# Kernel optimization log

Hardware: AMD Instinct MI355X
Metric: run time of the kernel (lower is better)

## Reference

```python
import jax, jax.numpy as jnp
import numpy as np

N_NODES = 100000
N_EDGES = 1600000
IN_DIM, HID_DIM, OUT_DIM = 512, 64, 32


def _gcn_conv(x, row, col, W, b, n):
    # GCNConv: h = x W; out[v] = sum_{(u,v)} norm(u,v) * h[u] + b
    # deg computed on destination (col) with self-loops already included.
    deg = jax.ops.segment_sum(jnp.ones_like(col, dtype=x.dtype), col, num_segments=n)
    dinv = jnp.where(deg > 0, jax.lax.rsqrt(deg), 0.0)
    norm = dinv[row] * dinv[col]                      # [E]
    h = x @ W                                          # [N, out]
    msg = h[row] * norm[:, None]                       # [E, out] gather
    out = jax.ops.segment_sum(msg, col, num_segments=n)  # scatter-add
    return out + b


def setup_inputs() -> dict:
    key = jax.random.key(0)
    k1, k2, k3, k4 = jax.random.split(key, 4)
    x = jax.random.normal(k1, (N_NODES, IN_DIM), dtype=jnp.float32)
    edge_index = jax.random.randint(k2, (2, N_EDGES), 0, N_NODES, dtype=jnp.int64)
    W1 = jax.random.normal(k3, (IN_DIM, HID_DIM), dtype=jnp.float32) / np.sqrt(IN_DIM)
    b1 = jnp.zeros((HID_DIM,), dtype=jnp.float32)
    W2 = jax.random.normal(k4, (HID_DIM, OUT_DIM), dtype=jnp.float32) / np.sqrt(HID_DIM)
    b2 = jnp.zeros((OUT_DIM,), dtype=jnp.float32)
    return {"x": x, "edge_index": edge_index, "W1": W1, "b1": b1, "W2": W2, "b2": b2}


def reference(x, edge_index, W1, b1, W2, b2):
    n = x.shape[0]
    # add self-loops (PyG GCNConv default add_self_loops=True)
    loop = jnp.arange(n, dtype=edge_index.dtype)
    row = jnp.concatenate([edge_index[0], loop])
    col = jnp.concatenate([edge_index[1], loop])
    h = _gcn_conv(x, row, col, W1, b1, n)
    h = jax.nn.relu(h)
    # dropout is identity in eval mode (training=False)
    h = _gcn_conv(h, row, col, W2, b2, n)
    return jax.nn.log_softmax(h, axis=1)
```

## Files before the change

### kernel.cpp

```cpp
#include <hip/hip_runtime.h>
#include <hip/hip_fp16.h>


#define IN_DIM 512
#define HID    64
#define OUTD   32

typedef __attribute__((ext_vector_type(8))) short bf16x8;
typedef __attribute__((ext_vector_type(4))) float floatx4;
typedef __attribute__((ext_vector_type(4))) unsigned short ushort4v;
typedef __attribute__((ext_vector_type(8))) unsigned short ushort8v;

__device__ __forceinline__ unsigned short f2bf(float f) {
    unsigned int u = __float_as_uint(f);
    unsigned int r = (u + 0x7fffu + ((u >> 16) & 1u)) >> 16;
    return (unsigned short)r;
}
__device__ __forceinline__ float bf2f(unsigned short h) {
    return __uint_as_float(((unsigned int)h) << 16);
}

__device__ __forceinline__ float4 ld4h(const __half* p) {
    uint2 u = *(const uint2*)(p);
    __half2 a = *(__half2*)&u.x, b = *(__half2*)&u.y;
    float2 fa = __half22float2(a), fb = __half22float2(b);
    return make_float4(fa.x, fa.y, fb.x, fb.y);
}

__device__ __forceinline__ int eidx(const int* idx32, long long e, int is64) {
    if (is64) { const long long* p = (const long long*)idx32; return (int)p[e]; }
    return idx32[e];
}

__global__ void k_init(const float* __restrict__ W1,
                       unsigned short* __restrict__ W1t_hi,
                       unsigned short* __restrict__ W1t_lo,
                       const int* __restrict__ idx, int* __restrict__ flag,
                       int* __restrict__ cnt, int N) {
    int t = blockIdx.x * blockDim.x + threadIdx.x;
    if (t == 0) {
        int z = (idx[1] == 0) & (idx[3] == 0) & (idx[5] == 0) & (idx[7] == 0);
        *flag = z;
    }
    if (t < N) cnt[t] = 0;
    if (t < 64 * 512) {
        int n = t >> 9, k = t & 511;
        float v = W1[k * HID + n];
        unsigned short h = f2bf(v);
        W1t_hi[t] = h;
        W1t_lo[t] = f2bf(v - bf2f(h));
    }
}

__global__ void k_count(const int* __restrict__ idx, const int* __restrict__ flag,
                        int* __restrict__ cnt, int E) {
    int e = blockIdx.x * blockDim.x + threadIdx.x;
    if (e >= E) return;
    const int is64 = *flag;
    int c = eidx(idx, (long long)E + e, is64);
    atomicAdd(&cnt[c], 1);
}

__global__ void k_scanA(const int* __restrict__ cnt, int* __restrict__ rowptr,
                        int* __restrict__ part, float* __restrict__ dinv, int N) {
    __shared__ int s[256];
    const int t = threadIdx.x;
    const int i = blockIdx.x * 256 + t;
    int v = (i < N) ? cnt[i] : 0;
    if (i < N) dinv[i] = rsqrtf((float)(1 + v));
    s[t] = v;
    __syncthreads();
#pragma unroll
    for (int off = 1; off < 256; off <<= 1) {
        int x = (t >= off) ? s[t - off] : 0;
        __syncthreads();
        s[t] += x;
        __syncthreads();
    }
    if (i < N) rowptr[i] = s[t] - v;
    if (t == 255) part[blockIdx.x] = s[255];
}

__global__ void k_scanB(const int* __restrict__ part, int* __restrict__ partex, int nb) {
    __shared__ int s[1024];
    const int t = threadIdx.x;
    int v = (t < nb) ? part[t] : 0;
    s[t] = v;
    __syncthreads();
#pragma unroll
    for (int off = 1; off < 1024; off <<= 1) {
        int x = (t >= off) ? s[t - off] : 0;
        __syncthreads();
        s[t] += x;
        __syncthreads();
    }
    partex[t] = s[t] - v;
}

__global__ void k_scanC(int* __restrict__ rowptr, const int* __restrict__ partex,
                        int N, int E) {
    const int i = blockIdx.x * blockDim.x + threadIdx.x;
    if (i < N) rowptr[i] += partex[i >> 8];
    if (i == 0) rowptr[N] = E;
}

__global__ void k_place(const int* __restrict__ idx, const int* __restrict__ flag,
                        int* __restrict__ cnt, const int* __restrict__ rowptr,
                        int* __restrict__ src, int E) {
    int e = blockIdx.x * blockDim.x + threadIdx.x;
    if (e >= E) return;
    const int is64 = *flag;
    int r = eidx(idx, e, is64);
    int c = eidx(idx, (long long)E + e, is64);
    int ofs = atomicAdd(&cnt[c], -1) - 1;
    src[rowptr[c] + ofs] = r;
}

__launch_bounds__(256)
__global__ void k_gemm1_mfma(const float* __restrict__ x,
                             const unsigned short* __restrict__ Wt_hi,
                             const unsigned short* __restrict__ Wt_lo,
                             const float* __restrict__ dinv,
                             __half* __restrict__ g1, int N) {
    __shared__ unsigned short xs_hi[64 * 72];
    __shared__ unsigned short xs_lo[64 * 72];
    __shared__ unsigned short ws_hi[64 * 72];
    __shared__ unsigned short ws_lo[64 * 72];

    const int t = threadIdx.x;
    const int lane = t & 63;
    const int w = t >> 6;
    const int m = lane & 15;
    const int quad = lane >> 4;
    const int row_base = blockIdx.x * 64;

    const floatx4 zero = {0.0f, 0.0f, 0.0f, 0.0f};
    floatx4 acc[4] = {zero, zero, zero, zero};

    for (int kc = 0; kc < IN_DIM; kc += 64) {
        {
            const int kq = (t & 15) * 4;
#pragma unroll
            for (int p = 0; p < 4; ++p) {
                int rl = (t >> 4) + p * 16;
                int row = row_base + rl;
                if (row > N - 1) row = N - 1;
                float4 v = *(const float4*)(x + (size_t)row * IN_DIM + kc + kq);
                ushort4v hi, lo;
                hi.x = f2bf(v.x); lo.x = f2bf(v.x - bf2f(hi.x));
                hi.y = f2bf(v.y); lo.y = f2bf(v.y - bf2f(hi.y));
                hi.z = f2bf(v.z); lo.z = f2bf(v.z - bf2f(hi.z));
                hi.w = f2bf(v.w); lo.w = f2bf(v.w - bf2f(hi.w));
                *(ushort4v*)&xs_hi[rl * 72 + kq] = hi;
                *(ushort4v*)&xs_lo[rl * 72 + kq] = lo;
            }
        }
        {
            const int nl = t >> 2;
            const int q = (t & 3) * 16;
            const unsigned short* ph = Wt_hi + (size_t)nl * IN_DIM + kc + q;
            const unsigned short* pl = Wt_lo + (size_t)nl * IN_DIM + kc + q;
            *(ushort8v*)&ws_hi[nl * 72 + q]     = *(const ushort8v*)(ph);
            *(ushort8v*)&ws_hi[nl * 72 + q + 8] = *(const ushort8v*)(ph + 8);
            *(ushort8v*)&ws_lo[nl * 72 + q]     = *(const ushort8v*)(pl);
            *(ushort8v*)&ws_lo[nl * 72 + q + 8] = *(const ushort8v*)(pl + 8);
        }
        __syncthreads();
#pragma unroll
        for (int ks = 0; ks < 2; ++ks) {
            const int ko = ks * 32 + quad * 8;
            bf16x8 a_hi = *(const bf16x8*)&xs_hi[(w * 16 + m) * 72 + ko];
            bf16x8 a_lo = *(const bf16x8*)&xs_lo[(w * 16 + m) * 72 + ko];
#pragma unroll
            for (int nt = 0; nt < 4; ++nt) {
                bf16x8 b_hi = *(const bf16x8*)&ws_hi[(nt * 16 + m) * 72 + ko];
                bf16x8 b_lo = *(const bf16x8*)&ws_lo[(nt * 16 + m) * 72 + ko];
                acc[nt] = __builtin_amdgcn_mfma_f32_16x16x32_bf16(a_hi, b_hi, acc[nt], 0, 0, 0);
                acc[nt] = __builtin_amdgcn_mfma_f32_16x16x32_bf16(a_lo, b_hi, acc[nt], 0, 0, 0);
                acc[nt] = __builtin_amdgcn_mfma_f32_16x16x32_bf16(a_hi, b_lo, acc[nt], 0, 0, 0);
            }
        }
        __syncthreads();
    }
#pragma unroll
    for (int r = 0; r < 4; ++r) {
        const int row = row_base + w * 16 + quad * 4 + r;
        if (row < N) {
            const float dv = dinv[row];
#pragma unroll
            for (int nt = 0; nt < 4; ++nt)
                g1[(size_t)row * HID + nt * 16 + m] = __float2half(acc[nt][r] * dv);
        }
    }
}

__launch_bounds__(256)
__global__ void k_agg1_gemm2(const int* __restrict__ rowptr, const int* __restrict__ src,
                             const __half* __restrict__ g1, const float* __restrict__ W2,
                             const float* __restrict__ b1, const float* __restrict__ dinv,
                             __half* __restrict__ g2, int N) {
    __shared__ float w2s[HID * OUTD];
    __shared__ float hs[16][HID];
    __shared__ float sdv[16];

    const int t = threadIdx.x;
    for (int i = t; i < HID * OUTD; i += 256) w2s[i] = W2[i];

    const int wv = t >> 6, lane = t & 63;
    const int grp = lane >> 4;
    const int l16 = lane & 15;
    const int vl = wv * 4 + grp;
    const int v = blockIdx.x * 16 + vl;
    const int c0 = l16 * 4;

    if (v < N) {
        float4 acc = ld4h(g1 + (size_t)v * HID + c0);
        int i = rowptr[v];
        const int end = rowptr[v + 1];
        for (; i + 3 < end; i += 4) {
            int r0 = src[i], r1 = src[i + 1], r2 = src[i + 2], r3 = src[i + 3];
            float4 a0 = ld4h(g1 + (size_t)r0 * HID + c0);
            float4 a1 = ld4h(g1 + (size_t)r1 * HID + c0);
            float4 a2 = ld4h(g1 + (size_t)r2 * HID + c0);
            float4 a3 = ld4h(g1 + (size_t)r3 * HID + c0);
            acc.x += (a0.x + a1.x) + (a2.x + a3.x);
            acc.y += (a0.y + a1.y) + (a2.y + a3.y);
            acc.z += (a0.z + a1.z) + (a2.z + a3.z);
            acc.w += (a0.w + a1.w) + (a2.w + a3.w);
        }
        for (; i < end; ++i) {
            float4 a = ld4h(g1 + (size_t)src[i] * HID + c0);
            acc.x += a.x; acc.y += a.y; acc.z += a.z; acc.w += a.w;
        }
        const float dv = dinv[v];
        const float4 b = *(const float4*)(b1 + c0);
        float4 h;
        h.x = fmaxf(fmaf(dv, acc.x, b.x), 0.0f);
        h.y = fmaxf(fmaf(dv, acc.y, b.y), 0.0f);
        h.z = fmaxf(fmaf(dv, acc.z, b.z), 0.0f);
        h.w = fmaxf(fmaf(dv, acc.w, b.w), 0.0f);
        *(float4*)&hs[vl][c0] = h;
        if (l16 == 0) sdv[vl] = dv;
    }
    __syncthreads();
#pragma unroll
    for (int hh = 0; hh < 2; ++hh) {
        const int o = hh * 256 + t;
        const int vert = o >> 5;
        const int j = o & 31;
        const int gv = blockIdx.x * 16 + vert;
        if (gv < N) {
            float s = 0.0f;
#pragma unroll
            for (int k = 0; k < HID; ++k) s = fmaf(hs[vert][k], w2s[k * OUTD + j], s);
            g2[(size_t)gv * OUTD + j] = __float2half(s * sdv[vert]);
        }
    }
}

__global__ void k_out(const int* __restrict__ rowptr, const int* __restrict__ src,
                      const __half* __restrict__ g2, const float* __restrict__ b2,
                      const float* __restrict__ dinv, float* __restrict__ out, int N) {
    const int t = threadIdx.x;
    const int wv = t >> 6, lane = t & 63;
    const int grp = lane >> 3;
    const int l8 = lane & 7;
    const int v = blockIdx.x * 32 + wv * 8 + grp;
    if (v >= N) return;
    const int c0 = l8 * 4;

    float4 acc = ld4h(g2 + (size_t)v * OUTD + c0);
    int i = rowptr[v];
    const int end = rowptr[v + 1];
    for (; i + 3 < end; i += 4) {
        int r0 = src[i], r1 = src[i + 1], r2 = src[i + 2], r3 = src[i + 3];
        float4 a0 = ld4h(g2 + (size_t)r0 * OUTD + c0);
        float4 a1 = ld4h(g2 + (size_t)r1 * OUTD + c0);
        float4 a2 = ld4h(g2 + (size_t)r2 * OUTD + c0);
        float4 a3 = ld4h(g2 + (size_t)r3 * OUTD + c0);
        acc.x += (a0.x + a1.x) + (a2.x + a3.x);
        acc.y += (a0.y + a1.y) + (a2.y + a3.y);
        acc.z += (a0.z + a1.z) + (a2.z + a3.z);
        acc.w += (a0.w + a1.w) + (a2.w + a3.w);
    }
    for (; i < end; ++i) {
        float4 a = ld4h(g2 + (size_t)src[i] * OUTD + c0);
        acc.x += a.x; acc.y += a.y; acc.z += a.z; acc.w += a.w;
    }
    const float dv = dinv[v];
    const float4 b = *(const float4*)(b2 + c0);
    float4 z;
    z.x = fmaf(dv, acc.x, b.x);
    z.y = fmaf(dv, acc.y, b.y);
    z.z = fmaf(dv, acc.z, b.z);
    z.w = fmaf(dv, acc.w, b.w);
    float m = fmaxf(fmaxf(z.x, z.y), fmaxf(z.z, z.w));
#pragma unroll
    for (int d = 1; d < 8; d <<= 1) m = fmaxf(m, __shfl_xor(m, d, 64));
    float s = expf(z.x - m) + expf(z.y - m) + expf(z.z - m) + expf(z.w - m);
#pragma unroll
    for (int d = 1; d < 8; d <<= 1) s += __shfl_xor(s, d, 64);
    const float ml = m + logf(s);
    float4 o;
    o.x = z.x - ml; o.y = z.y - ml; o.z = z.z - ml; o.w = z.w - ml;
    *(float4*)(out + (size_t)v * OUTD + c0) = o;
}

extern "C" void kernel_launch(void* const* d_in, const int* in_sizes, int n_in,
                              void* d_out, int out_size, void* d_ws, size_t ws_size,
                              hipStream_t stream) {
    const float* x   = (const float*)d_in[0];
    const int*   idx = (const int*)d_in[1];
    const float* W1  = (const float*)d_in[2];
    const float* b1  = (const float*)d_in[3];
    const float* W2  = (const float*)d_in[4];
    const float* b2  = (const float*)d_in[5];
    float* out = (float*)d_out;

    const int N = in_sizes[0] / IN_DIM;
    const int E = in_sizes[1] / 2;

    unsigned short* W1t_hi = (unsigned short*)d_ws;
    unsigned short* W1t_lo = W1t_hi + 64 * 512;
    int* cnt    = (int*)(W1t_lo + 64 * 512);
    int* rowptr = cnt + N;
    int* part   = rowptr + (N + 4);
    int* partex = part + 1024;
    int* srcA   = partex + 1024;
    int* flag   = srcA + E;
    float* dinv = (float*)(flag + 4);
    __half* g1  = (__half*)(dinv + N);
    __half* g2  = g1 + (size_t)N * HID;

    const int B = 256;
    const int nb = (N + 255) / 256;

    k_init<<<(N + B - 1) / B, B, 0, stream>>>(W1, W1t_hi, W1t_lo, idx, flag, cnt, N);
    k_count<<<(E + B - 1) / B, B, 0, stream>>>(idx, flag, cnt, E);
    k_scanA<<<nb, 256, 0, stream>>>(cnt, rowptr, part, dinv, N);
    k_scanB<<<1, 1024, 0, stream>>>(part, partex, nb);
    k_scanC<<<nb, 256, 0, stream>>>(rowptr, partex, N, E);
    k_place<<<(E + B - 1) / B, B, 0, stream>>>(idx, flag, cnt, rowptr, srcA, E);

    k_gemm1_mfma<<<(N + 63) / 64, 256, 0, stream>>>(x, W1t_hi, W1t_lo, dinv, g1, N);
    k_agg1_gemm2<<<(N + 15) / 16, 256, 0, stream>>>(rowptr, srcA, g1, W2, b1, dinv, g2, N);
    k_out<<<(N + 31) / 32, B, 0, stream>>>(rowptr, srcA, g2, b2, dinv, out, N);
}
```

Measured before the change: 547.5 us.

## Sort vertices by in-degree to balance aggregation work across wavefronts

Builds a degree histogram and a counting-sort permutation of vertices by in-degree, then has both aggregation kernels process vertices in permuted order. Groups that share a wavefront then have similar neighbor counts, which is meant to cut divergence and load imbalance in the per-vertex gather loops. This costs two extra small kernels plus atomics, and output writes become scattered rather than contiguous.

```diff
diff --git a/kernel.cpp b/kernel.cpp
--- a/kernel.cpp
+++ b/kernel.cpp
@@ -36,12 +36,13 @@
                        unsigned short* __restrict__ W1t_hi,
                        unsigned short* __restrict__ W1t_lo,
                        const int* __restrict__ idx, int* __restrict__ flag,
-                       int* __restrict__ cnt, int N) {
+                       int* __restrict__ cnt, int* __restrict__ hist, int N) {
     int t = blockIdx.x * blockDim.x + threadIdx.x;
     if (t == 0) {
         int z = (idx[1] == 0) & (idx[3] == 0) & (idx[5] == 0) & (idx[7] == 0);
         *flag = z;
     }
+    if (t < 256) hist[t] = 0;
     if (t < N) cnt[t] = 0;
     if (t < 64 * 512) {
         int n = t >> 9, k = t & 511;
@@ -98,10 +99,57 @@
 }
 
 __global__ void k_scanC(int* __restrict__ rowptr, const int* __restrict__ partex,
+                        const int* __restrict__ cnt, int* __restrict__ hist,
                         int N, int E) {
-    const int i = blockIdx.x * blockDim.x + threadIdx.x;
-    if (i < N) rowptr[i] += partex[i >> 8];
+    __shared__ int lh[256];
+    const int t = threadIdx.x;
+    const int i = blockIdx.x * 256 + t;
+    lh[t] = 0;
+    __syncthreads();
+    if (i < N) {
+        rowptr[i] += partex[i >> 8];
+        atomicAdd(&lh[min(cnt[i], 255)], 1);
+    }
     if (i == 0) rowptr[N] = E;
+    __syncthreads();
+    int c = lh[t];
+    if (c) atomicAdd(&hist[t], c);
+}
+
+__global__ void k_binscan(const int* __restrict__ hist, int* __restrict__ binofs) {
+    __shared__ int s[256];
+    const int t = threadIdx.x;
+    int v = hist[t];
+    s[t] = v;
+    __syncthreads();
+#pragma unroll
+    for (int off = 1; off < 256; off <<= 1) {
+        int x = (t >= off) ? s[t - off] : 0;
+        __syncthreads();
+        s[t] += x;
+        __syncthreads();
+    }
+    binofs[t] = s[t] - v;
+}
+
+__global__ void k_permplace(const int* __restrict__ cnt, int* __restrict__ binofs,
+                            int* __restrict__ perm, int N) {
+    __shared__ int lh[256];
+    __shared__ int lbase[256];
+    const int t = threadIdx.x;
+    const int v = blockIdx.x * 256 + t;
+    lh[t] = 0;
+    __syncthreads();
+    int d = 0, my = 0;
+    if (v < N) {
+        d = min(cnt[v], 255);
+        my = atomicAdd(&lh[d], 1);
+    }
+    __syncthreads();
+    int c = lh[t];
+    if (c) lbase[t] = atomicAdd(&binofs[t], c);
+    __syncthreads();
+    if (v < N) perm[lbase[d] + my] = v;
 }
 
 __global__ void k_place(const int* __restrict__ idx, const int* __restrict__ flag,
@@ -196,12 +244,14 @@
 
 __launch_bounds__(256)
 __global__ void k_agg1_gemm2(const int* __restrict__ rowptr, const int* __restrict__ src,
+                             const int* __restrict__ perm,
                              const __half* __restrict__ g1, const float* __restrict__ W2,
                              const float* __restrict__ b1, const float* __restrict__ dinv,
                              __half* __restrict__ g2, int N) {
     __shared__ float w2s[HID * OUTD];
     __shared__ float hs[16][HID];
     __shared__ float sdv[16];
+    __shared__ int   svid[16];
 
     const int t = threadIdx.x;
     for (int i = t; i < HID * OUTD; i += 256) w2s[i] = W2[i];
@@ -210,10 +260,11 @@
     const int grp = lane >> 4;
     const int l16 = lane & 15;
     const int vl = wv * 4 + grp;
-    const int v = blockIdx.x * 16 + vl;
+    const int idxv = blockIdx.x * 16 + vl;
+    const int v = (idxv < N) ? perm[idxv] : -1;
     const int c0 = l16 * 4;
 
-    if (v < N) {
+    if (v >= 0) {
         float4 acc = ld4h(g1 + (size_t)v * HID + c0);
         int i = rowptr[v];
         const int end = rowptr[v + 1];
@@ -240,7 +291,9 @@
         h.z = fmaxf(fmaf(dv, acc.z, b.z), 0.0f);
         h.w = fmaxf(fmaf(dv, acc.w, b.w), 0.0f);
         *(float4*)&hs[vl][c0] = h;
-        if (l16 == 0) sdv[vl] = dv;
+        if (l16 == 0) { sdv[vl] = dv; svid[vl] = v; }
+    } else if (l16 == 0) {
+        svid[vl] = -1;
     }
     __syncthreads();
 #pragma unroll
@@ -248,8 +301,8 @@
         const int o = hh * 256 + t;
         const int vert = o >> 5;
         const int j = o & 31;
-        const int gv = blockIdx.x * 16 + vert;
-        if (gv < N) {
+        const int gv = svid[vert];
+        if (gv >= 0) {
             float s = 0.0f;
 #pragma unroll
             for (int k = 0; k < HID; ++k) s = fmaf(hs[vert][k], w2s[k * OUTD + j], s);
@@ -259,14 +312,16 @@
 }
 
 __global__ void k_out(const int* __restrict__ rowptr, const int* __restrict__ src,
+                      const int* __restrict__ perm,
                       const __half* __restrict__ g2, const float* __restrict__ b2,
                       const float* __restrict__ dinv, float* __restrict__ out, int N) {
     const int t = threadIdx.x;
     const int wv = t >> 6, lane = t & 63;
     const int grp = lane >> 3;
     const int l8 = lane & 7;
-    const int v = blockIdx.x * 32 + wv * 8 + grp;
-    if (v >= N) return;
+    const int idxv = blockIdx.x * 32 + wv * 8 + grp;
+    if (idxv >= N) return;
+    const int v = perm[idxv];
     const int c0 = l8 * 4;
 
     float4 acc = ld4h(g2 + (size_t)v * OUTD + c0);
@@ -326,7 +381,10 @@
     int* rowptr = cnt + N;
     int* part   = rowptr + (N + 4);
     int* partex = part + 1024;
-    int* srcA   = partex + 1024;
+    int* hist   = partex + 1024;
+    int* binofs = hist + 256;
+    int* perm   = binofs + 256;
+    int* srcA   = perm + N;
     int* flag   = srcA + E;
     float* dinv = (float*)(flag + 4);
     __half* g1  = (__half*)(dinv + N);
@@ -335,14 +393,16 @@
     const int B = 256;
     const int nb = (N + 255) / 256;
 
-    k_init<<<(N + B - 1) / B, B, 0, stream>>>(W1, W1t_hi, W1t_lo, idx, flag, cnt, N);
+    k_init<<<(N + B - 1) / B, B, 0, stream>>>(W1, W1t_hi, W1t_lo, idx, flag, cnt, hist, N);
     k_count<<<(E + B - 1) / B, B, 0, stream>>>(idx, flag, cnt, E);
     k_scanA<<<nb, 256, 0, stream>>>(cnt, rowptr, part, dinv, N);
     k_scanB<<<1, 1024, 0, stream>>>(part, partex, nb);
-    k_scanC<<<nb, 256, 0, stream>>>(rowptr, partex, N, E);
+    k_scanC<<<nb, 256, 0, stream>>>(rowptr, partex, cnt, hist, N, E);
+    k_binscan<<<1, 256, 0, stream>>>(hist, binofs);
+    k_permplace<<<nb, 256, 0, stream>>>(cnt, binofs, perm, N);
     k_place<<<(E + B - 1) / B, B, 0, stream>>>(idx, flag, cnt, rowptr, srcA, E);
 
     k_gemm1_mfma<<<(N + 63) / 64, 256, 0, stream>>>(x, W1t_hi, W1t_lo, dinv, g1, N);
-    k_agg1_gemm2<<<(N + 15) / 16, 256, 0, stream>>>(rowptr, srcA, g1, W2, b1, dinv, g2, N);
-    k_out<<<(N + 31) / 32, B, 0, stream>>>(rowptr, srcA, g2, b2, dinv, out, N);
-}
+    k_agg1_gemm2<<<(N + 15) / 16, 256, 0, stream>>>(rowptr, srcA, perm, g1, W2, b1, dinv, g2, N);
+    k_out<<<(N + 31) / 32, B, 0, stream>>>(rowptr, srcA, perm, g2, b2, dinv, out, N);
+}
```

Result: slower. 572.1 us (+4.5%).

## Load GEMM1 operands directly into registers and record edge offsets during counting

Applied to the files above, without the earlier changes.

The first-layer GEMM no longer stages x and W1 tiles through LDS. Each lane loads its own A fragment from global memory, converts it to bf16 hi/lo in registers, and reads B fragments straight from the pre-transposed weight arrays, so the block-wide barriers are gone. Separately, the count pass now stores each edge's atomic slot index, which lets the place pass drop its second round of atomics on the counters. The cost is an extra E-sized int buffer written and read back, and weight reads that now depend on L1/L2 caching instead of shared memory. Neighbour ordering within each row is now determined by the count pass's atomic order.

```diff
diff --git a/kernel.cpp b/kernel.cpp
--- a/kernel.cpp
+++ b/kernel.cpp
@@ -8,8 +8,6 @@
 
 typedef __attribute__((ext_vector_type(8))) short bf16x8;
 typedef __attribute__((ext_vector_type(4))) float floatx4;
-typedef __attribute__((ext_vector_type(4))) unsigned short ushort4v;
-typedef __attribute__((ext_vector_type(8))) unsigned short ushort8v;
 
 __device__ __forceinline__ unsigned short f2bf(float f) {
     unsigned int u = __float_as_uint(f);
@@ -53,12 +51,12 @@
 }
 
 __global__ void k_count(const int* __restrict__ idx, const int* __restrict__ flag,
-                        int* __restrict__ cnt, int E) {
+                        int* __restrict__ cnt, int* __restrict__ eofs, int E) {
     int e = blockIdx.x * blockDim.x + threadIdx.x;
     if (e >= E) return;
     const int is64 = *flag;
     int c = eidx(idx, (long long)E + e, is64);
-    atomicAdd(&cnt[c], 1);
+    eofs[e] = atomicAdd(&cnt[c], 1);
 }
 
 __global__ void k_scanA(const int* __restrict__ cnt, int* __restrict__ rowptr,
@@ -105,28 +103,21 @@
 }
 
 __global__ void k_place(const int* __restrict__ idx, const int* __restrict__ flag,
-                        int* __restrict__ cnt, const int* __restrict__ rowptr,
+                        const int* __restrict__ eofs, const int* __restrict__ rowptr,
                         int* __restrict__ src, int E) {
     int e = blockIdx.x * blockDim.x + threadIdx.x;
     if (e >= E) return;
     const int is64 = *flag;
     int r = eidx(idx, e, is64);
     int c = eidx(idx, (long long)E + e, is64);
-    int ofs = atomicAdd(&cnt[c], -1) - 1;
-    src[rowptr[c] + ofs] = r;
-}
-
-__launch_bounds__(256)
+    src[rowptr[c] + eofs[e]] = r;
+}
+
 __global__ void k_gemm1_mfma(const float* __restrict__ x,
                              const unsigned short* __restrict__ Wt_hi,
                              const unsigned short* __restrict__ Wt_lo,
                              const float* __restrict__ dinv,
                              __half* __restrict__ g1, int N) {
-    __shared__ unsigned short xs_hi[64 * 72];
-    __shared__ unsigned short xs_lo[64 * 72];
-    __shared__ unsigned short ws_hi[64 * 72];
-    __shared__ unsigned short ws_lo[64 * 72];
-
     const int t = threadIdx.x;
     const int lane = t & 63;
     const int w = t >> 6;
@@ -134,53 +125,43 @@
     const int quad = lane >> 4;
     const int row_base = blockIdx.x * 64;
 
+    int arow = row_base + w * 16 + m;
+    if (arow > N - 1) arow = N - 1;
+    const float* xp = x + (size_t)arow * IN_DIM + quad * 8;
+    const unsigned short* wh = Wt_hi + (size_t)m * IN_DIM + quad * 8;
+    const unsigned short* wl = Wt_lo + (size_t)m * IN_DIM + quad * 8;
+
     const floatx4 zero = {0.0f, 0.0f, 0.0f, 0.0f};
     floatx4 acc[4] = {zero, zero, zero, zero};
 
     for (int kc = 0; kc < IN_DIM; kc += 64) {
-        {
-            const int kq = (t & 15) * 4;
-#pragma unroll
-            for (int p = 0; p < 4; ++p) {
-                int rl = (t >> 4) + p * 16;
-                int row = row_base + rl;
-                if (row > N - 1) row = N - 1;
-                float4 v = *(const float4*)(x + (size_t)row * IN_DIM + kc + kq);
-                ushort4v hi, lo;
-                hi.x = f2bf(v.x); lo.x = f2bf(v.x - bf2f(hi.x));
-                hi.y = f2bf(v.y); lo.y = f2bf(v.y - bf2f(hi.y));
-                hi.z = f2bf(v.z); lo.z = f2bf(v.z - bf2f(hi.z));
-                hi.w = f2bf(v.w); lo.w = f2bf(v.w - bf2f(hi.w));
-                *(ushort4v*)&xs_hi[rl * 72 + kq] = hi;
-                *(ushort4v*)&xs_lo[rl * 72 + kq] = lo;
+#pragma unroll
+        for (int ks = 0; ks < 2; ++ks) {
+            const int ko = kc + ks * 32;
+            float4 v0 = *(const float4*)(xp + ko);
+            float4 v1 = *(const float4*)(xp + ko + 4);
+            bf16x8 a_hi, a_lo;
+            {
+                unsigned short h;
+                h = f2bf(v0.x); a_hi[0] = (short)h; a_lo[0] = (short)f2bf(v0.x - bf2f(h));
+                h = f2bf(v0.y); a_hi[1] = (short)h; a_lo[1] = (short)f2bf(v0.y - bf2f(h));
+                h = f2bf(v0.z); a_hi[2] = (short)h; a_lo[2] = (short)f2bf(v0.z - bf2f(h));
+                h = f2bf(v0.w); a_hi[3] = (short)h; a_lo[3] = (short)f2bf(v0.w - bf2f(h));
+                h = f2bf(v1.x); a_hi[4] = (short)h; a_lo[4] = (short)f2bf(v1.x - bf2f(h));
+                h = f2bf(v1.y); a_hi[5] = (short)h; a_lo[5] = (short)f2bf(v1.y - bf2f(h));
+                h = f2bf(v1.z); a_hi[6] = (short)h; a_lo[6] = (short)f2bf(v1.z - bf2f(h));
+                h = f2bf(v1.w); a_hi[7] = (short)h; a_lo[7] = (short)f2bf(v1.w - bf2f(h));
             }
-        }
-        {
-            const int nl = t >> 2;
-            const int q = (t & 3) * 16;
-            const unsigned short* ph = Wt_hi + (size_t)nl * IN_DIM + kc + q;
-            const unsigned short* pl = Wt_lo + (size_t)nl * IN_DIM + kc + q;
-            *(ushort8v*)&ws_hi[nl * 72 + q]     = *(const ushort8v*)(ph);
-            *(ushort8v*)&ws_hi[nl * 72 + q + 8] = *(const ushort8v*)(ph + 8);
-            *(ushort8v*)&ws_lo[nl * 72 + q]     = *(const ushort8v*)(pl);
-            *(ushort8v*)&ws_lo[nl * 72 + q + 8] = *(const ushort8v*)(pl + 8);
-        }
-        __syncthreads();
-#pragma unroll
-        for (int ks = 0; ks < 2; ++ks) {
-            const int ko = ks * 32 + quad * 8;
-            bf16x8 a_hi = *(const bf16x8*)&xs_hi[(w * 16 + m) * 72 + ko];
-            bf16x8 a_lo = *(const bf16x8*)&xs_lo[(w * 16 + m) * 72 + ko];
 #pragma unroll
             for (int nt = 0; nt < 4; ++nt) {
-                bf16x8 b_hi = *(const bf16x8*)&ws_hi[(nt * 16 + m) * 72 + ko];
-                bf16x8 b_lo = *(const bf16x8*)&ws_lo[(nt * 16 + m) * 72 + ko];
+                const size_t wo = (size_t)(nt * 16) * IN_DIM + ko;
+                bf16x8 b_hi = *(const bf16x8*)(wh + wo);
+                bf16x8 b_lo = *(const bf16x8*)(wl + wo);
                 acc[nt] = __builtin_amdgcn_mfma_f32_16x16x32_bf16(a_hi, b_hi, acc[nt], 0, 0, 0);
                 acc[nt] = __builtin_amdgcn_mfma_f32_16x16x32_bf16(a_lo, b_hi, acc[nt], 0, 0, 0);
                 acc[nt] = __builtin_amdgcn_mfma_f32_16x16x32_bf16(a_hi, b_lo, acc[nt], 0, 0, 0);
             }
         }
-        __syncthreads();
     }
 #pragma unroll
     for (int r = 0; r < 4; ++r) {
@@ -327,7 +308,8 @@
     int* part   = rowptr + (N + 4);
     int* partex = part + 1024;
     int* srcA   = partex + 1024;
-    int* flag   = srcA + E;
+    int* eofs   = srcA + E;
+    int* flag   = eofs + E;
     float* dinv = (float*)(flag + 4);
     __half* g1  = (__half*)(dinv + N);
     __half* g2  = g1 + (size_t)N * HID;
@@ -336,11 +318,11 @@
     const int nb = (N + 255) / 256;
 
     k_init<<<(N + B - 1) / B, B, 0, stream>>>(W1, W1t_hi, W1t_lo, idx, flag, cnt, N);
-    k_count<<<(E + B - 1) / B, B, 0, stream>>>(idx, flag, cnt, E);
+    k_count<<<(E + B - 1) / B, B, 0, stream>>>(idx, flag, cnt, eofs, E);
     k_scanA<<<nb, 256, 0, stream>>>(cnt, rowptr, part, dinv, N);
     k_scanB<<<1, 1024, 0, stream>>>(part, partex, nb);
     k_scanC<<<nb, 256, 0, stream>>>(rowptr, partex, N, E);
-    k_place<<<(E + B - 1) / B, B, 0, stream>>>(idx, flag, cnt, rowptr, srcA, E);
+    k_place<<<(E + B - 1) / B, B, 0, stream>>>(idx, flag, eofs, rowptr, srcA, E);
 
     k_gemm1_mfma<<<(N + 63) / 64, 256, 0, stream>>>(x, W1t_hi, W1t_lo, dinv, g1, N);
     k_agg1_gemm2<<<(N + 15) / 16, 256, 0, stream>>>(rowptr, srcA, g1, W2, b1, dinv, g2, N);
```

New measurement: 574.8 us. +5.0%, slower.
